# Optimization experiments

Measured on AMD Instinct MI355X. Metric: run time of the kernel, lower is better.

Reference implementation:

```python
import jax, jax.numpy as jnp
import numpy as np

B = 32768
HID = 64
IU = np.triu_indices(9)  # 45 upper-triangular (incl. diagonal) entries of a 9x9 matrix
DIAG = np.arange(9)


def setup_inputs() -> dict:
    key = jax.random.key(0)
    ks = jax.random.split(key, 12)
    return {
        "x": jax.random.normal(ks[0], (B, 1, 9, 7), jnp.float32),
        "adj": jax.random.randint(ks[1], (B, 45), 0, 2, jnp.int32),
        "context": jax.random.normal(ks[2], (B, 1, 9, 5), jnp.float32),
        # DenseGCNConv(7, 7): linear weight + bias
        "gcn_W": jax.random.normal(ks[3], (7, 7), jnp.float32) * 0.3,
        "gcn_b": jax.random.normal(ks[4], (7,), jnp.float32) * 0.05,
        # context_net Linear(45, 63)
        "ctx_W": jax.random.normal(ks[5], (45, 63), jnp.float32) * 0.15,
        "ctx_b": jax.random.normal(ks[6], (63,), jnp.float32) * 0.05,
        # three 1x1 convs: 2->64, 64->64, 64->2 (weights stored [out, in])
        "W1": jax.random.normal(ks[7], (HID, 2), jnp.float32) * 0.5,
        "b1": jnp.zeros((HID,), jnp.float32),
        "W2": jax.random.normal(ks[8], (HID, HID), jnp.float32) * 0.12,
        "b2": jnp.zeros((HID,), jnp.float32),
        "W3": jax.random.normal(ks[9], (2, HID), jnp.float32) * 0.12,
        "b3": jnp.zeros((2,), jnp.float32),
    }


def reference(x, adj, context, gcn_W, gcn_b, ctx_W, ctx_b, W1, b1, W2, b2, W3, b3):
    Bn = x.shape[0]
    # scatter 45 edge values into the upper triangle of a [B,9,9] adjacency, binarize
    A = jnp.zeros((Bn, 9, 9), jnp.float32).at[:, IU[0], IU[1]].set(adj.astype(jnp.float32))
    A = (A > 0.0).astype(jnp.float32)
    # DenseGCNConv: add self-loops (diag := 1), symmetric degree normalization
    A = A.at[:, DIAG, DIAG].set(1.0)
    d = jnp.maximum(A.sum(-1), 1.0) ** -0.5  # [B,9]
    An = d[:, :, None] * A * d[:, None, :]
    z = x[:, 0]  # [B,9,7]
    z = jnp.einsum('bnm,bmf->bnf', An, z @ gcn_W) + gcn_b  # [B,9,7]
    # context MLP: flatten -> Linear(45,63) -> ReLU -> reshape (9,7)
    c = jax.nn.relu(context.reshape(Bn, 1, 45) @ ctx_W + ctx_b).reshape(Bn, 1, 9, 7)
    h = jnp.concatenate([z[:, None], c], axis=1)  # [B,2,9,7]
    # 1x1 conv stack == per-pixel channel GEMMs
    h = jax.nn.relu(jnp.einsum('bchw,oc->bohw', h, W1) + b1[:, None, None])
    h = jax.nn.relu(jnp.einsum('bchw,oc->bohw', h, W2) + b2[:, None, None])
    return jnp.einsum('bchw,oc->bohw', h, W3) + b3[:, None, None]  # [B,2,9,7]
```

## Files before the change

### kernel.cpp

```cpp
#include <hip/hip_runtime.h>
#include <cstdint>

#define BLOCK_SIZE 256
#define NPOS 63
#define BPB  16

typedef __attribute__((ext_vector_type(8))) _Float16 f16x8;
typedef __attribute__((ext_vector_type(4))) float f32x4;
typedef __attribute__((ext_vector_type(4))) unsigned int uint4v;

__device__ __forceinline__ unsigned rne_f16(float a) {
    _Float16 h = (_Float16)a;
    return (unsigned)__builtin_bit_cast(unsigned short, h);
}
__device__ __forceinline__ unsigned pack_f16(float a, float b) {
    auto t = __builtin_amdgcn_cvt_pkrtz(a, b);
    return __builtin_bit_cast(unsigned, t);
}

__global__ __launch_bounds__(BLOCK_SIZE) void carnet_fused(
    const float* __restrict__ x,
    const int*   __restrict__ adj,
    const float* __restrict__ ctx,
    const float* __restrict__ gcn_W,
    const float* __restrict__ gcn_b,
    const float* __restrict__ ctx_W,
    const float* __restrict__ ctx_b,
    const float* __restrict__ W1,
    const float* __restrict__ b1,
    const float* __restrict__ W2,
    const float* __restrict__ b2,
    const float* __restrict__ W3,
    const float* __restrict__ b3,
    float* __restrict__ out,
    const int nbatch)
{
    __shared__ short sh2b[64 * 64];
    __shared__ float w3b2[192];

    const int t    = threadIdx.x;
    const int lane = t & 63;

    {
        const int r  = t >> 2;
        const int cq = t & 3;
        const float* wsrc = W2 + r * 64 + cq * 16;
        const float4 w0 = ((const float4*)wsrc)[0];
        const float4 w1 = ((const float4*)wsrc)[1];
        const float4 w2v = ((const float4*)wsrc)[2];
        const float4 w3v = ((const float4*)wsrc)[3];
        uint4v hA = { rne_f16(w0.x)  | (rne_f16(w0.y)  << 16),
                      rne_f16(w0.z)  | (rne_f16(w0.w)  << 16),
                      rne_f16(w1.x)  | (rne_f16(w1.y)  << 16),
                      rne_f16(w1.z)  | (rne_f16(w1.w)  << 16) };
        uint4v hB = { rne_f16(w2v.x) | (rne_f16(w2v.y) << 16),
                      rne_f16(w2v.z) | (rne_f16(w2v.w) << 16),
                      rne_f16(w3v.x) | (rne_f16(w3v.y) << 16),
                      rne_f16(w3v.z) | (rne_f16(w3v.w) << 16) };
        const int sA = ((2 * cq)     ^ (r & 7)) * 8;
        const int sB = ((2 * cq + 1) ^ (r & 7)) * 8;
        *(uint4v*)&sh2b[r * 64 + sA] = hA;
        *(uint4v*)&sh2b[r * 64 + sB] = hB;
        if (t < 192) w3b2[t] = (t < 128) ? W3[t] : b2[t - 128];
    }

    const int bbase = blockIdx.x * BPB + (t >> 6);
    int  bs[4];
    bool vld[4];
#pragma unroll
    for (int u = 0; u < 4; ++u) {
        const int braw = bbase + u * 4;
        vld[u] = (braw < nbatch);
        bs[u]  = __builtin_amdgcn_readfirstlane(vld[u] ? braw : (nbatch - 1));
    }

    const int p = lane < 63 ? lane : 62;
    const int n = p / 7;
    const int f = p - n * 7;
    const int snn = 9 * n - (n * (n - 1)) / 2 - n;

    uint64_t am[4];
#pragma unroll
    for (int u = 0; u < 4; ++u) {
        int av = 0;
        if (lane < 45) av = adj[bs[u] * 45 + lane];
        am[u] = __ballot(av != 0);
    }

    float d[4][9];
#pragma unroll
    for (int i = 0; i < 9; ++i) {
        const int s = 9 * i - (i * (i - 1)) / 2;
        const uint64_t mk = (1ull << (8 - i)) - 1ull;
#pragma unroll
        for (int u = 0; u < 4; ++u)
            d[u][i] = __frsqrt_rn((float)(1 + __popcll((am[u] >> (s + 1)) & mk)));
    }

    float yv[4] = {0.f, 0.f, 0.f, 0.f};
#pragma unroll
    for (int k = 0; k < 7; ++k) {
        const float g = gcn_W[k * 7 + f];
#pragma unroll
        for (int u = 0; u < 4; ++u)
            yv[u] = fmaf(x[bs[u] * 63 + n * 7 + k], g, yv[u]);
    }

    float zt[4] = {0.f, 0.f, 0.f, 0.f};
#pragma unroll
    for (int m = 0; m < 9; ++m) {
        int sh = snn + m;
        sh = sh < 0 ? 0 : sh;
        const bool up = (m > n);
#pragma unroll
        for (int u = 0; u < 4; ++u) {
            const float ym = __shfl(yv[u], m * 7 + f);
            const float tm = ((m == n) || (up && ((am[u] >> sh) & 1ull))) ? d[u][m] : 0.f;
            zt[u] = fmaf(tm, ym, zt[u]);
        }
    }
    const float gbf = gcn_b[f];
    float zv[4];
#pragma unroll
    for (int u = 0; u < 4; ++u) zv[u] = fmaf(d[u][n], zt[u], gbf);

    const float cbias = ctx_b[p];
    float c0[4] = {cbias, cbias, cbias, cbias};
    float c1[4] = {0.f, 0.f, 0.f, 0.f};
#pragma unroll
    for (int q = 0; q < 44; q += 2) {
        const float w0 = ctx_W[q * 63 + p];
        const float w1 = ctx_W[(q + 1) * 63 + p];
#pragma unroll
        for (int u = 0; u < 4; ++u) {
            c0[u] = fmaf(ctx[bs[u] * 45 + q],     w0, c0[u]);
            c1[u] = fmaf(ctx[bs[u] * 45 + q + 1], w1, c1[u]);
        }
    }
    const float w44 = ctx_W[44 * 63 + p];
    float cvv[4];
#pragma unroll
    for (int u = 0; u < 4; ++u) {
        c0[u] = fmaf(ctx[bs[u] * 45 + 44], w44, c0[u]);
        cvv[u] = fmaxf(c0[u] + c1[u], 0.f);
    }

    const int cl   = lane & 15;
    const int quad = lane >> 4;
    const int s0 = (quad ^ (cl & 7)) * 16;

    float2 wp0[8], wp1[8];
    float  bb0[8], bb1[8];
#pragma unroll
    for (int j = 0; j < 8; ++j) {
        const int o = quad * 8 + j;
        wp0[j] = *(const float2*)(W1 + 2 * o);
        bb0[j] = b1[o];
        wp1[j] = *(const float2*)(W1 + 2 * (o + 32));
        bb1[j] = b1[o + 32];
    }
    const float b30 = b3[0], b31 = b3[1];

    float* __restrict__ ob[4];
#pragma unroll
    for (int u = 0; u < 4; ++u) ob[u] = out + bs[u] * 126;

    const char* sh2bB_ = (const char*)sh2b;

    __syncthreads();

#pragma unroll 1
    for (int i = 0; i < 4; ++i) {
        float zm[4], cm[4];
#pragma unroll
        for (int u = 0; u < 4; ++u) {
            zm[u] = __shfl(zv[u],  i * 16 + cl);
            cm[u] = __shfl(cvv[u], i * 16 + cl);
        }

        f32x4 bq_[4];
#pragma unroll
        for (int k2 = 0; k2 < 4; ++k2) {
            int o = 128 + k2 * 16 + quad * 4;
            asm volatile("" : "+v"(o));
            bq_[k2] = *(const f32x4*)&w3b2[o];
        }

        f16x8 ah0[4], ah1[4];
#pragma unroll
        for (int u = 0; u < 4; ++u) {
            uint4v p0, p1;
#pragma unroll
            for (int jj = 0; jj < 4; ++jj) {
                float ha = fmaxf(fmaf(wp0[2*jj].x,   zm[u], fmaf(wp0[2*jj].y,   cm[u], bb0[2*jj])),   0.f);
                float hb = fmaxf(fmaf(wp0[2*jj+1].x, zm[u], fmaf(wp0[2*jj+1].y, cm[u], bb0[2*jj+1])), 0.f);
                p0[jj] = pack_f16(ha, hb);
                ha = fmaxf(fmaf(wp1[2*jj].x,   zm[u], fmaf(wp1[2*jj].y,   cm[u], bb1[2*jj])),   0.f);
                hb = fmaxf(fmaf(wp1[2*jj+1].x, zm[u], fmaf(wp1[2*jj+1].y, cm[u], bb1[2*jj+1])), 0.f);
                p1[jj] = pack_f16(ha, hb);
            }
            ah0[u] = __builtin_bit_cast(f16x8, p0);
            ah1[u] = __builtin_bit_cast(f16x8, p1);
        }

        f32x4 acc[4][4];
#pragma unroll
        for (int u = 0; u < 4; ++u)
#pragma unroll
            for (int k2 = 0; k2 < 4; ++k2)
                acc[u][k2] = bq_[k2];

#pragma unroll
        for (int nt = 0; nt < 4; ++nt) {
            int bo = cl * 128 + s0;
            asm volatile("" : "+v"(bo));
            const int bo2 = (cl * 128) | (s0 ^ 64);
            const f16x8 wf0 = *(const f16x8*)(sh2bB_ + bo  + nt * 2048);
            const f16x8 wf1 = *(const f16x8*)(sh2bB_ + bo2 + nt * 2048);
#pragma unroll
            for (int u = 0; u < 4; ++u) {
                acc[u][nt] = __builtin_amdgcn_mfma_f32_16x16x32_f16(wf0, ah0[u], acc[u][nt], 0, 0, 0);
                acc[u][nt] = __builtin_amdgcn_mfma_f32_16x16x32_f16(wf1, ah1[u], acc[u][nt], 0, 0, 0);
            }
        }

        f32x4 wa_[4], wb_[4];
#pragma unroll
        for (int k2 = 0; k2 < 4; ++k2) {
            int o = k2 * 16 + quad * 4;
            asm volatile("" : "+v"(o));
            wa_[k2] = *(const f32x4*)&w3b2[o];
            wb_[k2] = *(const f32x4*)&w3b2[64 + o];
        }

        const int pp = i * 16 + cl;
#pragma unroll
        for (int u = 0; u < 4; ++u) {
            float q0 = 0.f, q1 = 0.f;
#pragma unroll
            for (int k2 = 0; k2 < 4; ++k2) {
#pragma unroll
                for (int e = 0; e < 4; ++e) {
                    const float h = fmaxf(acc[u][k2][e], 0.f);
                    q0 = fmaf(h, wa_[k2][e], q0);
                    q1 = fmaf(h, wb_[k2][e], q1);
                }
            }
            q0 += __shfl_xor(q0, 16); q0 += __shfl_xor(q0, 32);
            q1 += __shfl_xor(q1, 16); q1 += __shfl_xor(q1, 32);
            if (quad == 0 && pp < NPOS && vld[u]) {
                ob[u][pp]        = q0 + b30;
                ob[u][NPOS + pp] = q1 + b31;
            }
        }
    }
}

extern "C" void kernel_launch(void* const* d_in, const int* in_sizes, int n_in,
                              void* d_out, int out_size, void* d_ws, size_t ws_size,
                              hipStream_t stream) {
    const float* x     = (const float*)d_in[0];
    const int*   adj   = (const int*)  d_in[1];
    const float* ctx   = (const float*)d_in[2];
    const float* gcn_W = (const float*)d_in[3];
    const float* gcn_b = (const float*)d_in[4];
    const float* ctx_W = (const float*)d_in[5];
    const float* ctx_b = (const float*)d_in[6];
    const float* W1    = (const float*)d_in[7];
    const float* b1    = (const float*)d_in[8];
    const float* W2    = (const float*)d_in[9];
    const float* b2    = (const float*)d_in[10];
    const float* W3    = (const float*)d_in[11];
    const float* b3    = (const float*)d_in[12];
    float* out = (float*)d_out;

    const int nbatch = in_sizes[1] / 45;
    const int grid = (nbatch + BPB - 1) / BPB;
    carnet_fused<<<grid, BLOCK_SIZE, 0, stream>>>(
        x, adj, ctx, gcn_W, gcn_b, ctx_W, ctx_b,
        W1, b1, W2, b2, W3, b3, out, nbatch);
}
```

Baseline: 165.3 us.

## Cut batches per wave to three and stage W1/b1 in shared memory

Each wave now handles three batch items instead of four, so a block covers 12 batches and more blocks launch. The W1 weights and b1 biases, which every thread used to hold in registers for the whole kernel, are copied into shared memory and reloaded inside the position loop. The aim is to lower register pressure and raise occupancy. The cost is extra LDS reads per iteration and less reuse of each MFMA weight fragment across batch items.

```diff
diff --git a/kernel.cpp b/kernel.cpp
--- a/kernel.cpp
+++ b/kernel.cpp
@@ -3,7 +3,8 @@
 
 #define BLOCK_SIZE 256
 #define NPOS 63
-#define BPB  16
+#define NB   3
+#define BPB  12
 
 typedef __attribute__((ext_vector_type(8))) _Float16 f16x8;
 typedef __attribute__((ext_vector_type(4))) float f32x4;
@@ -36,7 +37,7 @@
     const int nbatch)
 {
     __shared__ short sh2b[64 * 64];
-    __shared__ float w3b2[192];
+    __shared__ float wbuf[384];
 
     const int t    = threadIdx.x;
     const int lane = t & 63;
@@ -61,14 +62,24 @@
         const int sB = ((2 * cq + 1) ^ (r & 7)) * 8;
         *(uint4v*)&sh2b[r * 64 + sA] = hA;
         *(uint4v*)&sh2b[r * 64 + sB] = hB;
-        if (t < 192) w3b2[t] = (t < 128) ? W3[t] : b2[t - 128];
+        {
+            float v;
+            if (t < 128)      v = W3[t];
+            else if (t < 192) v = b2[t - 128];
+            else              v = W1[t - 192];
+            wbuf[t] = v;
+            if (t < 128) {
+                const int i2 = 256 + t;
+                wbuf[i2] = (i2 < 320) ? W1[i2 - 192] : b1[i2 - 320];
+            }
+        }
     }
 
     const int bbase = blockIdx.x * BPB + (t >> 6);
-    int  bs[4];
-    bool vld[4];
-#pragma unroll
-    for (int u = 0; u < 4; ++u) {
+    int  bs[NB];
+    bool vld[NB];
+#pragma unroll
+    for (int u = 0; u < NB; ++u) {
         const int braw = bbase + u * 4;
         vld[u] = (braw < nbatch);
         bs[u]  = __builtin_amdgcn_readfirstlane(vld[u] ? braw : (nbatch - 1));
@@ -79,68 +90,68 @@
     const int f = p - n * 7;
     const int snn = 9 * n - (n * (n - 1)) / 2 - n;
 
-    uint64_t am[4];
-#pragma unroll
-    for (int u = 0; u < 4; ++u) {
+    uint64_t am[NB];
+#pragma unroll
+    for (int u = 0; u < NB; ++u) {
         int av = 0;
         if (lane < 45) av = adj[bs[u] * 45 + lane];
         am[u] = __ballot(av != 0);
     }
 
-    float d[4][9];
+    float d[NB][9];
 #pragma unroll
     for (int i = 0; i < 9; ++i) {
         const int s = 9 * i - (i * (i - 1)) / 2;
         const uint64_t mk = (1ull << (8 - i)) - 1ull;
 #pragma unroll
-        for (int u = 0; u < 4; ++u)
+        for (int u = 0; u < NB; ++u)
             d[u][i] = __frsqrt_rn((float)(1 + __popcll((am[u] >> (s + 1)) & mk)));
     }
 
-    float yv[4] = {0.f, 0.f, 0.f, 0.f};
+    float yv[NB] = {0.f, 0.f, 0.f};
 #pragma unroll
     for (int k = 0; k < 7; ++k) {
         const float g = gcn_W[k * 7 + f];
 #pragma unroll
-        for (int u = 0; u < 4; ++u)
+        for (int u = 0; u < NB; ++u)
             yv[u] = fmaf(x[bs[u] * 63 + n * 7 + k], g, yv[u]);
     }
 
-    float zt[4] = {0.f, 0.f, 0.f, 0.f};
+    float zt[NB] = {0.f, 0.f, 0.f};
 #pragma unroll
     for (int m = 0; m < 9; ++m) {
         int sh = snn + m;
         sh = sh < 0 ? 0 : sh;
         const bool up = (m > n);
 #pragma unroll
-        for (int u = 0; u < 4; ++u) {
+        for (int u = 0; u < NB; ++u) {
             const float ym = __shfl(yv[u], m * 7 + f);
             const float tm = ((m == n) || (up && ((am[u] >> sh) & 1ull))) ? d[u][m] : 0.f;
             zt[u] = fmaf(tm, ym, zt[u]);
         }
     }
     const float gbf = gcn_b[f];
-    float zv[4];
-#pragma unroll
-    for (int u = 0; u < 4; ++u) zv[u] = fmaf(d[u][n], zt[u], gbf);
+    float zv[NB];
+#pragma unroll
+    for (int u = 0; u < NB; ++u) zv[u] = fmaf(d[u][n], zt[u], gbf);
 
     const float cbias = ctx_b[p];
-    float c0[4] = {cbias, cbias, cbias, cbias};
-    float c1[4] = {0.f, 0.f, 0.f, 0.f};
+    float c0[NB] = {cbias, cbias, cbias};
+    float c1[NB] = {0.f, 0.f, 0.f};
 #pragma unroll
     for (int q = 0; q < 44; q += 2) {
         const float w0 = ctx_W[q * 63 + p];
         const float w1 = ctx_W[(q + 1) * 63 + p];
 #pragma unroll
-        for (int u = 0; u < 4; ++u) {
+        for (int u = 0; u < NB; ++u) {
             c0[u] = fmaf(ctx[bs[u] * 45 + q],     w0, c0[u]);
             c1[u] = fmaf(ctx[bs[u] * 45 + q + 1], w1, c1[u]);
         }
     }
     const float w44 = ctx_W[44 * 63 + p];
-    float cvv[4];
-#pragma unroll
-    for (int u = 0; u < 4; ++u) {
+    float cvv[NB];
+#pragma unroll
+    for (int u = 0; u < NB; ++u) {
         c0[u] = fmaf(ctx[bs[u] * 45 + 44], w44, c0[u]);
         cvv[u] = fmaxf(c0[u] + c1[u], 0.f);
     }
@@ -149,21 +160,11 @@
     const int quad = lane >> 4;
     const int s0 = (quad ^ (cl & 7)) * 16;
 
-    float2 wp0[8], wp1[8];
-    float  bb0[8], bb1[8];
-#pragma unroll
-    for (int j = 0; j < 8; ++j) {
-        const int o = quad * 8 + j;
-        wp0[j] = *(const float2*)(W1 + 2 * o);
-        bb0[j] = b1[o];
-        wp1[j] = *(const float2*)(W1 + 2 * (o + 32));
-        bb1[j] = b1[o + 32];
-    }
     const float b30 = b3[0], b31 = b3[1];
 
-    float* __restrict__ ob[4];
-#pragma unroll
-    for (int u = 0; u < 4; ++u) ob[u] = out + bs[u] * 126;
+    float* __restrict__ ob[NB];
+#pragma unroll
+    for (int u = 0; u < NB; ++u) ob[u] = out + bs[u] * 126;
 
     const char* sh2bB_ = (const char*)sh2b;
 
@@ -171,44 +172,60 @@
 
 #pragma unroll 1
     for (int i = 0; i < 4; ++i) {
-        float zm[4], cm[4];
-#pragma unroll
-        for (int u = 0; u < 4; ++u) {
+        float zm[NB], cm[NB];
+#pragma unroll
+        for (int u = 0; u < NB; ++u) {
             zm[u] = __shfl(zv[u],  i * 16 + cl);
             cm[u] = __shfl(cvv[u], i * 16 + cl);
         }
 
-        f32x4 bq_[4];
+        f32x4 w1a[4], w1b[4], bbA2[2], bbB2[2];
+#pragma unroll
+        for (int jj = 0; jj < 4; ++jj) {
+            int o = 192 + quad * 16 + jj * 4;
+            asm volatile("" : "+v"(o));
+            w1a[jj] = *(const f32x4*)&wbuf[o];
+            int o2 = 256 + quad * 16 + jj * 4;
+            asm volatile("" : "+v"(o2));
+            w1b[jj] = *(const f32x4*)&wbuf[o2];
+        }
+#pragma unroll
+        for (int h = 0; h < 2; ++h) {
+            int o = 320 + quad * 8 + h * 4;
+            asm volatile("" : "+v"(o));
+            bbA2[h] = *(const f32x4*)&wbuf[o];
+            int o2 = 352 + quad * 8 + h * 4;
+            asm volatile("" : "+v"(o2));
+            bbB2[h] = *(const f32x4*)&wbuf[o2];
+        }
+
+        f16x8 ah0[NB], ah1[NB];
+#pragma unroll
+        for (int u = 0; u < NB; ++u) {
+            uint4v p0, p1;
+#pragma unroll
+            for (int jj = 0; jj < 4; ++jj) {
+                const int be = (jj & 1) * 2;
+                float ha = fmaxf(fmaf(w1a[jj][0], zm[u], fmaf(w1a[jj][1], cm[u], bbA2[jj >> 1][be])),     0.f);
+                float hb = fmaxf(fmaf(w1a[jj][2], zm[u], fmaf(w1a[jj][3], cm[u], bbA2[jj >> 1][be + 1])), 0.f);
+                p0[jj] = pack_f16(ha, hb);
+                ha = fmaxf(fmaf(w1b[jj][0], zm[u], fmaf(w1b[jj][1], cm[u], bbB2[jj >> 1][be])),     0.f);
+                hb = fmaxf(fmaf(w1b[jj][2], zm[u], fmaf(w1b[jj][3], cm[u], bbB2[jj >> 1][be + 1])), 0.f);
+                p1[jj] = pack_f16(ha, hb);
+            }
+            ah0[u] = __builtin_bit_cast(f16x8, p0);
+            ah1[u] = __builtin_bit_cast(f16x8, p1);
+        }
+
+        f32x4 acc[NB][4];
 #pragma unroll
         for (int k2 = 0; k2 < 4; ++k2) {
             int o = 128 + k2 * 16 + quad * 4;
             asm volatile("" : "+v"(o));
-            bq_[k2] = *(const f32x4*)&w3b2[o];
-        }
-
-        f16x8 ah0[4], ah1[4];
-#pragma unroll
-        for (int u = 0; u < 4; ++u) {
-            uint4v p0, p1;
-#pragma unroll
-            for (int jj = 0; jj < 4; ++jj) {
-                float ha = fmaxf(fmaf(wp0[2*jj].x,   zm[u], fmaf(wp0[2*jj].y,   cm[u], bb0[2*jj])),   0.f);
-                float hb = fmaxf(fmaf(wp0[2*jj+1].x, zm[u], fmaf(wp0[2*jj+1].y, cm[u], bb0[2*jj+1])), 0.f);
-                p0[jj] = pack_f16(ha, hb);
-                ha = fmaxf(fmaf(wp1[2*jj].x,   zm[u], fmaf(wp1[2*jj].y,   cm[u], bb1[2*jj])),   0.f);
-                hb = fmaxf(fmaf(wp1[2*jj+1].x, zm[u], fmaf(wp1[2*jj+1].y, cm[u], bb1[2*jj+1])), 0.f);
-                p1[jj] = pack_f16(ha, hb);
-            }
-            ah0[u] = __builtin_bit_cast(f16x8, p0);
-            ah1[u] = __builtin_bit_cast(f16x8, p1);
-        }
-
-        f32x4 acc[4][4];
-#pragma unroll
-        for (int u = 0; u < 4; ++u)
-#pragma unroll
-            for (int k2 = 0; k2 < 4; ++k2)
-                acc[u][k2] = bq_[k2];
+            const f32x4 bq = *(const f32x4*)&wbuf[o];
+#pragma unroll
+            for (int u = 0; u < NB; ++u) acc[u][k2] = bq;
+        }
 
 #pragma unroll
         for (int nt = 0; nt < 4; ++nt) {
@@ -218,7 +235,7 @@
             const f16x8 wf0 = *(const f16x8*)(sh2bB_ + bo  + nt * 2048);
             const f16x8 wf1 = *(const f16x8*)(sh2bB_ + bo2 + nt * 2048);
 #pragma unroll
-            for (int u = 0; u < 4; ++u) {
+            for (int u = 0; u < NB; ++u) {
                 acc[u][nt] = __builtin_amdgcn_mfma_f32_16x16x32_f16(wf0, ah0[u], acc[u][nt], 0, 0, 0);
                 acc[u][nt] = __builtin_amdgcn_mfma_f32_16x16x32_f16(wf1, ah1[u], acc[u][nt], 0, 0, 0);
             }
@@ -229,13 +246,13 @@
         for (int k2 = 0; k2 < 4; ++k2) {
             int o = k2 * 16 + quad * 4;
             asm volatile("" : "+v"(o));
-            wa_[k2] = *(const f32x4*)&w3b2[o];
-            wb_[k2] = *(const f32x4*)&w3b2[64 + o];
+            wa_[k2] = *(const f32x4*)&wbuf[o];
+            wb_[k2] = *(const f32x4*)&wbuf[64 + o];
         }
 
         const int pp = i * 16 + cl;
 #pragma unroll
-        for (int u = 0; u < 4; ++u) {
+        for (int u = 0; u < NB; ++u) {
             float q0 = 0.f, q1 = 0.f;
 #pragma unroll
             for (int k2 = 0; k2 < 4; ++k2) {
```

Result: faster. 154.6 us (-6.5%).
